# Kernel tuning notes

Measured on AMD Instinct MI355X. Metric: run time of the kernel, lower is better.

The kernel has to match this reference:

```python
import math
import jax, jax.numpy as jnp
from jax import lax
import numpy as np

B, H_IMG, W_IMG = 16, 512, 512
POOL, RATIO, SCALE = 23, 2, 0.25

def conv2d(x, w, b=None, stride=1, pad=0):
    y = lax.conv_general_dilated(x, w, (stride, stride), [(pad, pad), (pad, pad)],
                                 dimension_numbers=('NCHW', 'OIHW', 'NCHW'))
    return y if b is None else y + b[None, :, None, None]

def batchnorm(x, g, b, eps=1e-5):
    # training-mode BN (module is never put in eval mode): batch statistics
    m = x.mean((0, 2, 3), keepdims=True)
    v = x.var((0, 2, 3), keepdims=True)
    return g[None, :, None, None] * (x - m) * lax.rsqrt(v + eps) + b[None, :, None, None]

def maxpool(x, k, s, p=0):
    return lax.reduce_window(x, -jnp.inf, lax.max, (1, 1, k, k), (1, 1, s, s),
                             [(0, 0), (0, 0), (p, p), (p, p)])

def affine_grid(theta, H, W):
    # F.affine_grid, align_corners=False
    xs = (jnp.arange(W, dtype=jnp.float32) * 2 + 1) / W - 1
    ys = (jnp.arange(H, dtype=jnp.float32) * 2 + 1) / H - 1
    gx, gy = jnp.meshgrid(xs, ys)  # [H,W]
    base = jnp.stack([gx, gy, jnp.ones_like(gx)], axis=-1)  # [H,W,3]
    return base @ theta.T  # [H,W,2] -> (x,y) source coords

def grid_sample(imgs, grid):
    # bilinear, zero padding, align_corners=False; imgs [B,C,H,W], grid [H,W,2]
    _, C, H, W = imgs.shape
    ix = ((grid[..., 0] + 1) * W - 1) * 0.5
    iy = ((grid[..., 1] + 1) * H - 1) * 0.5
    x0, y0 = jnp.floor(ix), jnp.floor(iy)
    wa = (x0 + 1 - ix) * (y0 + 1 - iy)
    wb = (x0 + 1 - ix) * (iy - y0)
    wc = (ix - x0) * (y0 + 1 - iy)
    wd = (ix - x0) * (iy - y0)
    def gather(img, yy, xx):
        valid = (xx >= 0) & (xx < W) & (yy >= 0) & (yy < H)
        return img[:, jnp.clip(yy, 0, H - 1).astype(jnp.int32),
                      jnp.clip(xx, 0, W - 1).astype(jnp.int32)] * valid
    def one(img):
        return (gather(img, y0, x0) * wa + gather(img, y0 + 1, x0) * wb +
                gather(img, y0, x0 + 1) * wc + gather(img, y0 + 1, x0 + 1) * wd)
    return jax.vmap(one)(imgs)

def roialign(feat, ind, boxes):
    # torchvision ROIAlign(output=(23,23), spatial_scale=0.25, sampling_ratio=2, aligned=False)
    C, H, W = feat.shape[1:]
    x1, y1, x2, y2 = (boxes * SCALE).T
    bw = jnp.maximum(x2 - x1, 1.0) / POOL
    bh = jnp.maximum(y2 - y1, 1.0) / POOL
    off = (jnp.arange(RATIO, dtype=jnp.float32) + 0.5) / RATIO
    pos = (jnp.arange(POOL, dtype=jnp.float32)[:, None] + off[None, :]).reshape(-1)  # [46]
    ys = y1[:, None] + pos[None, :] * bh[:, None]  # [N,46]
    xs = x1[:, None] + pos[None, :] * bw[:, None]
    S = POOL * RATIO
    def one(img, yv, xv):
        empty = ((yv[:, None] < -1.0) | (yv[:, None] > H) |
                 (xv[None, :] < -1.0) | (xv[None, :] > W))  # [S,S]
        y = jnp.broadcast_to(jnp.clip(yv, 0.0, H - 1.0)[:, None], (S, S))
        x = jnp.broadcast_to(jnp.clip(xv, 0.0, W - 1.0)[None, :], (S, S))
        y0f, x0f = jnp.floor(y), jnp.floor(x)
        y0 = y0f.astype(jnp.int32); x0 = x0f.astype(jnp.int32)
        y1i = jnp.minimum(y0 + 1, H - 1); x1i = jnp.minimum(x0 + 1, W - 1)
        ly, lx = y - y0f, x - x0f
        hy, hx = 1.0 - ly, 1.0 - lx
        v = (img[:, y0, x0] * (hy * hx) + img[:, y0, x1i] * (hy * lx) +
             img[:, y1i, x0] * (ly * hx) + img[:, y1i, x1i] * (ly * lx))
        v = jnp.where(empty[None], 0.0, v)
        return v.reshape(C, POOL, RATIO, POOL, RATIO).mean((2, 4))
    return jax.vmap(one)(feat[ind], ys, xs)  # [N,C,23,23]

def forward(x, box, stem_w, stem_g, stem_b, conv1_w, conv1_b, bn1_g, bn1_b,
            conv2_w, conv2_b, fc1_w, fc1_b, head_w, head_b):
    x = x.transpose(0, 3, 1, 2)  # NHWC -> NCHW
    # resnet stem (7x7/2 conv + BN + ReLU + 3x3/2 maxpool): 64 ch @ stride 4
    f = maxpool(jax.nn.relu(batchnorm(conv2d(x, stem_w, stride=2, pad=3), stem_g, stem_b)), 3, 2, 1)
    Bc, C, H, W = f.shape
    a = -5 * math.pi / 180
    theta1 = jnp.array([[math.cos(a), math.sin(-a), 0.0], [math.sin(a), math.cos(a), 0.0]], jnp.float32)
    a = 5 * math.pi / 180
    theta2 = jnp.array([[math.cos(a), math.sin(-a), 0.0], [math.sin(a), math.cos(a), 0.0]], jnp.float32)
    xt1 = grid_sample(f, affine_grid(theta1, H, W))
    xt2 = grid_sample(f, affine_grid(theta2, H, W))
    ind = jnp.arange(Bc, dtype=jnp.int32)
    b7 = box.reshape(Bc, 7, 4)
    # focus1..focus7 on f, channel order matches torch.cat((f1..f7), dim=1)
    boxes7 = b7.transpose(1, 0, 2).reshape(7 * Bc, 4)
    f7 = roialign(f, jnp.tile(ind, 7), boxes7).reshape(7, Bc, C, POOL, POOL)
    f7 = f7.transpose(1, 0, 2, 3, 4).reshape(Bc, 7 * C, POOL, POOL)
    b1, b2 = b7[:, 0], b7[:, 1]
    f8 = roialign(xt1, ind, b1)
    f9 = roialign(xt1, ind, b2)
    f10 = roialign(xt2, ind, b1)
    f11 = roialign(xt2, ind, b2)
    h = jnp.concatenate([f7, f8, f9, f10, f11], axis=1)  # [B,704,23,23]
    h = maxpool(jax.nn.relu(batchnorm(conv2d(h, conv1_w, conv1_b), bn1_g, bn1_b)), 2, 2)  # [B,64,10,10]
    h = jax.nn.relu(conv2d(h, conv2_w, conv2_b))  # [B,32,8,8]
    h = h.reshape(Bc, 32 * 8 * 8)
    h = jax.nn.relu(h @ fc1_w.T + fc1_b)
    return jnp.tanh(h @ head_w.T + head_b)  # [B,12]

def setup_inputs() -> dict:
    key = jax.random.key(0)
    ks = jax.random.split(key, 8)
    x = jax.random.normal(ks[0], (B, H_IMG, W_IMG, 3), jnp.float32)
    xy = jax.random.uniform(ks[1], (B, 7, 2), jnp.float32, 0.0, 300.0)
    wh = jax.random.uniform(ks[2], (B, 7, 2), jnp.float32, 50.0, 200.0)
    box = jnp.concatenate([xy, xy + wh], axis=-1).reshape(B, 28)
    def w(k, shape, fan_in):
        return jax.random.normal(k, shape, jnp.float32) / np.float32(np.sqrt(fan_in))
    return dict(
        x=x, box=box,
        stem_w=w(ks[3], (64, 3, 7, 7), 3 * 49),
        stem_g=jnp.ones((64,), jnp.float32), stem_b=jnp.zeros((64,), jnp.float32),
        conv1_w=w(ks[4], (64, 704, 3, 3), 704 * 9), conv1_b=jnp.zeros((64,), jnp.float32),
        bn1_g=jnp.ones((64,), jnp.float32), bn1_b=jnp.zeros((64,), jnp.float32),
        conv2_w=w(ks[5], (32, 64, 3, 3), 64 * 9), conv2_b=jnp.zeros((32,), jnp.float32),
        fc1_w=w(ks[6], (128, 2048), 2048), fc1_b=jnp.zeros((128,), jnp.float32),
        head_w=w(ks[7], (12, 128), 128), head_b=jnp.zeros((12,), jnp.float32),
    )

def reference(x, box, stem_w, stem_g, stem_b, conv1_w, conv1_b, bn1_g, bn1_b,
              conv2_w, conv2_b, fc1_w, fc1_b, head_w, head_b):
    return forward(x, box, stem_w, stem_g, stem_b, conv1_w, conv1_b, bn1_g, bn1_b,
                   conv2_w, conv2_b, fc1_w, fc1_b, head_w, head_b)
```

## Files before the change

### kernel.cpp

```cpp
#include <hip/hip_runtime.h>
#include <hip/hip_bf16.h>


#define C5 0.9961946980917455f
#define S5 0.08715574274765817f

typedef __attribute__((ext_vector_type(8))) short short8;
typedef __attribute__((ext_vector_type(4))) float f32x4;

typedef __attribute__((address_space(3))) ushort lds_ushort;
typedef const __attribute__((address_space(1))) ushort gbl_ushort;

__device__ __forceinline__ ushort f2bf_bits(float v) {
    __hip_bfloat16 b = __float2bfloat16(v);
    ushort u;
    __builtin_memcpy(&u, &b, 2);
    return u;
}
__device__ __forceinline__ float bfbits2f(ushort u) {
    __hip_bfloat16 b;
    __builtin_memcpy(&b, &u, 2);
    return __bfloat162float(b);
}

__global__ __launch_bounds__(256) void k_cvtall(const float* __restrict__ x,
                                                ushort* __restrict__ xbf,
                                                const float* __restrict__ w1,
                                                __hip_bfloat16* __restrict__ w1b,
                                                const float* __restrict__ sw,
                                                __hip_bfloat16* __restrict__ w2b,
                                                float* __restrict__ stats_raw) {
    const int bx = blockIdx.x;
    if (bx < 12627) {
        const int t = bx * 256 + threadIdx.x;
        if (t >= 3232480) return;
        const int n = t / 202020;
        const int r = t - n * 202020;
        const int row = r / 390, col = r - row * 390;
        const int ih = row - 3;
        float4 v = {0.f, 0.f, 0.f, 0.f};
        if ((unsigned)ih < 512u && col >= 3 && col <= 386)
            v = *(const float4*)(x + (size_t)n * 786432 + (size_t)ih * 1536 + 4 * col - 12);
        uint2 p;
        p.x = (uint)f2bf_bits(v.x) | ((uint)f2bf_bits(v.y) << 16);
        p.y = (uint)f2bf_bits(v.z) | ((uint)f2bf_bits(v.w) << 16);
        *(uint2*)(xbf + 4 * (size_t)t) = p;
    } else {
        const int t = (bx - 12627) * 256 + threadIdx.x;
        if (t < 405504) {
            w1b[t] = __float2bfloat16(w1[t]);
        } else if (t < 417792) {
            const int e = t - 405504;
            const int oc = e / 192, k = e - oc * 192;
            const int kh = k / 24, u = k - kh * 24;
            float v = 0.f;
            if (u >= 3 && kh < 7) {
                int tt = u - 3;
                int kw = tt / 3, ci = tt - kw * 3;
                v = sw[oc * 147 + ci * 49 + kh * 7 + kw];
            }
            w2b[e] = __float2bfloat16(v);
        } else if (t < 417920) {
            stats_raw[t - 417792] = 0.f;
        }
    }
}

__global__ __launch_bounds__(64, 4) void k_stem(const ushort* __restrict__ xbf,
                                                const ushort* __restrict__ w2b,
                                                __hip_bfloat16* __restrict__ out) {
    __shared__ __align__(16) ushort lds[4608];
    const int bx = blockIdx.x;
    const int gi = ((bx & 7) << 11) + (bx >> 3);
    const int wq = gi & 3;
    const int oh = (gi >> 2) & 255;
    const int n  = gi >> 10;
    const int lane = threadIdx.x;
    const int quad = lane >> 4, m = lane & 15;
    const int p0 = wq * 64;

    {
        const ushort* src = xbf + (size_t)n * 808080 + (size_t)(oh * 2) * 1560 + 6 * p0;
        if (lane < 51) {
#pragma unroll
            for (int row = 0; row < 8; row++)
                __builtin_amdgcn_global_load_lds((gbl_ushort*)(src + row * 1560 + lane * 8),
                                                 (lds_ushort*)(lds + row * 416 + lane * 8),
                                                 16, 0, 0);
        }
    }
    asm volatile("s_waitcnt vmcnt(0)" ::: "memory");
    __builtin_amdgcn_sched_barrier(0);

    f32x4 acc[4][4] = {};
#pragma unroll
    for (int ks = 0; ks < 6; ks++) {
        const int g   = ks * 4 + quad;
        const int kh  = g / 3;
        const int gi2 = g - kh * 3;
        const uint* rr = (const uint*)lds + kh * 208 + 4 * gi2;
        short8 b[4];
#pragma unroll
        for (int nt = 0; nt < 4; nt++) {
            const uint* q = rr + 3 * (nt * 16 + m);
            uint4 t = (uint4){q[0], q[1], q[2], q[3]};
            __builtin_memcpy(&b[nt], &t, 16);
        }
        const int ko = ks * 32 + quad * 8;
#pragma unroll
        for (int mt = 0; mt < 4; mt++) {
            const short8 a = *(const short8*)(w2b + (size_t)(mt * 16 + m) * 192 + ko);
#pragma unroll
            for (int nt = 0; nt < 4; nt++)
                acc[mt][nt] = __builtin_amdgcn_mfma_f32_16x16x32_bf16(a, b[nt], acc[mt][nt], 0, 0, 0);
        }
    }

#pragma unroll
    for (int mt = 0; mt < 4; mt++)
#pragma unroll
        for (int nt = 0; nt < 4; nt++)
#pragma unroll
            for (int r = 0; r < 4; r++)
                lds[(mt * 16 + quad * 4 + r) * 72 + nt * 16 + m] = f2bf_bits(acc[mt][nt][r]);

    ushort* outb = (ushort*)out + (size_t)n * 64 * 65536 + oh * 256 + p0;
    const int ocl = lane >> 3, ch = lane & 7;
#pragma unroll
    for (int p = 0; p < 8; p++) {
        const int oc = p * 8 + ocl;
        uint4 v = *(const uint4*)&lds[oc * 72 + ch * 8];
        *(uint4*)(outb + (size_t)oc * 65536 + ch * 8) = v;
    }
}

__global__ __launch_bounds__(256) void k_sumstem(const ushort* __restrict__ stem,
                                                 float* __restrict__ stats_raw) {
    const int c = blockIdx.x >> 3, s = blockIdx.x & 7;
    const int tid = threadIdx.x;
    const uint4* b0 = (const uint4*)(stem + ((size_t)(s * 2) * 64 + c) * 65536);
    const uint4* b1 = (const uint4*)(stem + ((size_t)(s * 2 + 1) * 64 + c) * 65536);
    float sum = 0.f, sq = 0.f;
    for (int i = tid; i < 8192; i += 256) {
        uint4 v0 = b0[i], v1 = b1[i];
#pragma unroll
        for (int k = 0; k < 4; k++) {
            uint u0 = ((const uint*)&v0)[k], u1 = ((const uint*)&v1)[k];
            float a0 = __uint_as_float(u0 << 16);
            float a1 = __uint_as_float(u0 & 0xffff0000u);
            float a2 = __uint_as_float(u1 << 16);
            float a3 = __uint_as_float(u1 & 0xffff0000u);
            sum += a0 + a1 + a2 + a3;
            sq = fmaf(a0, a0, fmaf(a1, a1, fmaf(a2, a2, fmaf(a3, a3, sq))));
        }
    }
#pragma unroll
    for (int off = 32; off; off >>= 1) {
        sum += __shfl_xor(sum, off, 64);
        sq  += __shfl_xor(sq, off, 64);
    }
    __shared__ float shS[4], shQ[4];
    if ((tid & 63) == 0) { shS[tid >> 6] = sum; shQ[tid >> 6] = sq; }
    __syncthreads();
    if (tid == 0) {
        atomicAdd(&stats_raw[c * 2],     shS[0] + shS[1] + shS[2] + shS[3]);
        atomicAdd(&stats_raw[c * 2 + 1], shQ[0] + shQ[1] + shQ[2] + shQ[3]);
    }
}

__global__ __launch_bounds__(256) void k_bn1stats(const float* __restrict__ c1,
                                                  const float* __restrict__ gamma,
                                                  const float* __restrict__ beta,
                                                  float* __restrict__ stats1) {
    const int c = blockIdx.x;
    const int tid = threadIdx.x;
    float s = 0.f, ss = 0.f;
    for (int e = tid; e < 7056; e += 256) {
        int n = e / 441, p = e - n * 441;
        float v = c1[(n * 64 + c) * 441 + p];
        s += v; ss += v * v;
    }
    __shared__ float sh[8], sh2[8];
#pragma unroll
    for (int off = 32; off; off >>= 1) {
        s += __shfl_xor(s, off, 64);
        ss += __shfl_xor(ss, off, 64);
    }
    if ((tid & 63) == 0) { sh[tid >> 6] = s; sh2[tid >> 6] = ss; }
    __syncthreads();
    if (tid == 0) {
        s = sh[0] + sh[1] + sh[2] + sh[3];
        ss = sh2[0] + sh2[1] + sh2[2] + sh2[3];
        const float inv_n = 1.f / 7056.f;
        float mn = s * inv_n;
        float var = ss * inv_n - mn * mn;
        float a = gamma[c] * rsqrtf(var + 1e-5f);
        stats1[c] = a;
        stats1[64 + c] = beta[c] - mn * a;
    }
}

__global__ __launch_bounds__(256) void k_bnpool(const __hip_bfloat16* __restrict__ sin_,
                                                const float* __restrict__ stats_raw,
                                                const float* __restrict__ gamma,
                                                const float* __restrict__ beta,
                                                float* __restrict__ f) {
    const int idx = blockIdx.x * 256 + threadIdx.x;
    const int pwg = idx & 15;
    const int ph = (idx >> 4) & 127;
    const int c = (idx >> 11) & 63;
    const int n = idx >> 17;
    const int pw0 = pwg * 8;
    const float inv_n = 1.f / 1048576.f;
    const float S = stats_raw[c * 2], Q = stats_raw[c * 2 + 1];
    const float mn = S * inv_n;
    const float var = Q * inv_n - mn * mn;
    const float a = gamma[c] * rsqrtf(var + 1e-5f);
    const float b = beta[c] - mn * a;
    const uint* base = (const uint*)((const ushort*)sin_ + (size_t)(n * 64 + c) * 65536);

    float colmax[17];
#pragma unroll
    for (int k = 0; k < 17; k++) colmax[k] = -1e30f;

    const int r0 = ph * 2 - 1;
#pragma unroll
    for (int dr = 0; dr < 3; dr++) {
        const int r = r0 + dr;
        const bool rv = (unsigned)r < 256u;
        uint d[9];
        const uint* rp = base + r * 128 + pw0 - 1;
#pragma unroll
        for (int j = 0; j < 9; j++)
            d[j] = (rv && (pw0 > 0 || j > 0)) ? rp[j] : 0u;
#pragma unroll
        for (int j = 0; j < 9; j++) {
            float vhi = a * bfbits2f((ushort)(d[j] >> 16)) + b;
            colmax[2 * j] = rv ? fmaxf(colmax[2 * j], vhi) : colmax[2 * j];
            if (j > 0) {
                float vlo = a * bfbits2f((ushort)(d[j] & 0xFFFFu)) + b;
                colmax[2 * j - 1] = rv ? fmaxf(colmax[2 * j - 1], vlo) : colmax[2 * j - 1];
            }
        }
    }
    if (pw0 == 0) colmax[0] = -1e30f;

    float o[8];
#pragma unroll
    for (int i = 0; i < 8; i++)
        o[i] = fmaxf(fmaxf(colmax[2 * i], fmaxf(colmax[2 * i + 1], colmax[2 * i + 2])), 0.f);
    float* fp = f + (size_t)(n * 64 + c) * 16384 + ph * 128 + pw0;
    *(float4*)fp       = (float4){o[0], o[1], o[2], o[3]};
    *(float4*)(fp + 4) = (float4){o[4], o[5], o[6], o[7]};
}

__device__ __forceinline__ float gs_pad(const float* band, int ry0g,
                                        float ix, float iy) {
    float x0f = floorf(ix), y0f = floorf(iy);
    float lx = ix - x0f, ly = iy - y0f;
    float hx = 1.f - lx, hy = 1.f - ly;
    const int base = ((int)y0f - ry0g) * 144 + (int)x0f + 8;
    return band[base] * (hx * hy) + band[base + 144] * (hx * ly)
         + band[base + 1] * (lx * hy) + band[base + 145] * (lx * ly);
}

__global__ __launch_bounds__(256, 3) void k_gridsample2(const float* __restrict__ f,
                                                        float* __restrict__ xt1,
                                                        float* __restrict__ xt2) {
    __shared__ float band[78 * 144];
    const int bx = blockIdx.x;
    const int half = bx & 1;
    const int img_i = bx >> 1;
    const int h0 = half * 64;
    const int ry0g = half ? 57 : -7;
    const float* img = f + (size_t)img_i * 16384;
    const int tid = threadIdx.x;
    for (int e = tid; e < 78 * 36; e += 256) {
        const int r = e / 36, q = e - r * 36;
        const int gr = ry0g + r;
        float4 v = {0.f, 0.f, 0.f, 0.f};
        if ((unsigned)gr < 128u && q >= 2 && q <= 33)
            v = *(const float4*)(img + gr * 128 + 4 * q - 8);
        ((float4*)band)[e] = v;
    }
    __syncthreads();

    float* o1 = xt1 + (size_t)img_i * 16384 + h0 * 128;
    float* o2 = xt2 + (size_t)img_i * 16384 + h0 * 128;
    for (int e = tid; e < 8192; e += 256) {
        const int h = h0 + (e >> 7);
        const int w = e & 127;
        float gx = (2 * w + 1) * (1.f / 128.f) - 1.f;
        float gy = (2 * h + 1) * (1.f / 128.f) - 1.f;
        float g0a = C5 * gx + S5 * gy,  g1a = -S5 * gx + C5 * gy;
        float g0b = C5 * gx - S5 * gy,  g1b =  S5 * gx + C5 * gy;
        o1[e] = gs_pad(band, ry0g, ((g0a + 1.f) * 128.f - 1.f) * 0.5f,
                                   ((g1a + 1.f) * 128.f - 1.f) * 0.5f);
        o2[e] = gs_pad(band, ry0g, ((g0b + 1.f) * 128.f - 1.f) * 0.5f,
                                   ((g1b + 1.f) * 128.f - 1.f) * 0.5f);
    }
}

__global__ __launch_bounds__(256) void k_roialign(const float* __restrict__ f,
                                                  const float* __restrict__ xt1,
                                                  const float* __restrict__ xt2,
                                                  const float* __restrict__ box,
                                                  __hip_bfloat16* __restrict__ h) {
    __shared__ float reg[52 * 53];
    const int bx = blockIdx.x;
    const int job = bx % 11;
    const int nc = bx / 11;
    const int c = nc & 63;
    const int n = nc >> 6;
    int j, cbase;
    const float* src;
    if (job < 7)      { j = job;     cbase = job * 64;             src = f;   }
    else if (job < 9) { j = job - 7; cbase = 448 + (job - 7) * 64; src = xt1; }
    else              { j = job - 9; cbase = 576 + (job - 9) * 64; src = xt2; }
    const float* bp = box + n * 28 + j * 4;
    const float x1 = bp[0] * 0.25f, y1 = bp[1] * 0.25f;
    const float x2 = bp[2] * 0.25f, y2 = bp[3] * 0.25f;
    const float bw = fmaxf(x2 - x1, 1.f) * (1.f / 23.f);
    const float bh = fmaxf(y2 - y1, 1.f) * (1.f / 23.f);

    const int ry0 = (int)floorf(fminf(fmaxf(y1 + 0.25f * bh, 0.f), 127.f));
    int ry1 = min((int)floorf(fminf(fmaxf(y1 + 22.75f * bh, 0.f), 127.f)) + 1, 127);
    ry1 = min(ry1, ry0 + 51);
    const int rx0 = (int)floorf(fminf(fmaxf(x1 + 0.25f * bw, 0.f), 127.f));
    int rx1 = min((int)floorf(fminf(fmaxf(x1 + 22.75f * bw, 0.f), 127.f)) + 1, 127);
    rx1 = min(rx1, rx0 + 51);
    const int RH = ry1 - ry0 + 1, RW = rx1 - rx0 + 1;

    const float* img = src + (size_t)(n * 64 + c) * 16384;
    const int tid = threadIdx.x;
    const int lane = tid & 63, wv = tid >> 6;
    for (int r = wv; r < RH; r += 4)
        if (lane < RW)
            reg[r * 53 + lane] = img[(ry0 + r) * 128 + rx0 + lane];
    __syncthreads();

    __hip_bfloat16* hb = h + (size_t)(n * 704 + cbase + c) * 529;
    for (int pp = tid; pp < 529; pp += 256) {
        const int ph = pp / 23, pw = pp - ph * 23;
        float sum = 0.f;
#pragma unroll
        for (int s = 0; s < 4; s++) {
            const int r1 = s >> 1, r2 = s & 1;
            const float yv = y1 + (ph + r1 * 0.5f + 0.25f) * bh;
            const float xv = x1 + (pw + r2 * 0.5f + 0.25f) * bw;
            const bool ok = !(yv < -1.f || yv > 128.f || xv < -1.f || xv > 128.f);
            float y = fminf(fmaxf(yv, 0.f), 127.f);
            float x = fminf(fmaxf(xv, 0.f), 127.f);
            float y0f = floorf(y), x0f = floorf(x);
            int y0 = (int)y0f, x0 = (int)x0f;
            int iy0 = y0 - ry0, ix0 = x0 - rx0;
            int iy1 = min(y0 + 1, 127) - ry0, ix1 = min(x0 + 1, 127) - rx0;
            float ly = y - y0f, lx = x - x0f;
            float hy = 1.f - ly, hx = 1.f - lx;
            const float sc = ok ? 1.f : 0.f;
            sum += sc * (reg[iy0 * 53 + ix0] * (hy * hx) + reg[iy0 * 53 + ix1] * (hy * lx)
                       + reg[iy1 * 53 + ix0] * (ly * hx) + reg[iy1 * 53 + ix1] * (ly * lx));
        }
        hb[pp] = __float2bfloat16(sum * 0.25f);
    }
}

__global__ __launch_bounds__(256) void k_conv1m(const ushort* __restrict__ hb,
                                                const ushort* __restrict__ w1b,
                                                float* __restrict__ c1p) {
    __shared__ __align__(16) ushort Bs[2][2][32][40];
    const int bx = blockIdx.x;
    const int pt = bx % 17;
    const int n  = (bx / 17) & 15;
    const int s  = bx / 272;
    const int tid = threadIdx.x;
    const int w = tid >> 6, lane = tid & 63;
    const int quad = lane >> 4, m = lane & 15;
    const int kbase = s * 704;
    const int posb = pt * 32;
    const size_t hb_n = (size_t)n * 704 * 529;
    f32x4 acc0 = {0.f, 0.f, 0.f, 0.f};
    f32x4 acc1 = {0.f, 0.f, 0.f, 0.f};
    const ushort* wrow = w1b + (size_t)(w * 16 + m) * 6336;

    int ep[8], ek[8], epos[8];
#pragma unroll
    for (int i = 0; i < 8; i++) {
        const int e = tid + 256 * i;
        ep[i] = e >> 10; ek[i] = (e >> 5) & 31; epos[i] = e & 31;
    }
    ushort rbuf[8];
#pragma unroll
    for (int i = 0; i < 8; i++) {
        const int k = kbase + ep[i] * 32 + ek[i];
        const int ci = k / 9, tap = k - ci * 9;
        const int kh = tap / 3, kw = tap - kh * 3;
        rbuf[i] = hb[hb_n + (size_t)ci * 529 + kh * 23 + kw + posb + epos[i]];
    }
#pragma unroll
    for (int i = 0; i < 8; i++) Bs[0][ep[i]][epos[i]][ek[i]] = rbuf[i];

    for (int it = 0; it < 11; it++) {
        __syncthreads();
        const int cur = it & 1;
        if (it < 10) {
            const int k0 = kbase + (it + 1) * 64;
#pragma unroll
            for (int i = 0; i < 8; i++) {
                const int k = k0 + ep[i] * 32 + ek[i];
                const int ci = k / 9, tap = k - ci * 9;
                const int kh = tap / 3, kw = tap - kh * 3;
                rbuf[i] = hb[hb_n + (size_t)ci * 529 + kh * 23 + kw + posb + epos[i]];
            }
        }
        const int k0 = kbase + it * 64;
        const short8 a0  = *(const short8*)(wrow + k0 + quad * 8);
        const short8 a1  = *(const short8*)(wrow + k0 + 32 + quad * 8);
        const short8 b00 = *(const short8*)&Bs[cur][0][m][quad * 8];
        const short8 b01 = *(const short8*)&Bs[cur][0][16 + m][quad * 8];
        const short8 b10 = *(const short8*)&Bs[cur][1][m][quad * 8];
        const short8 b11 = *(const short8*)&Bs[cur][1][16 + m][quad * 8];
        acc0 = __builtin_amdgcn_mfma_f32_16x16x32_bf16(a0, b00, acc0, 0, 0, 0);
        acc1 = __builtin_amdgcn_mfma_f32_16x16x32_bf16(a0, b01, acc1, 0, 0, 0);
        acc0 = __builtin_amdgcn_mfma_f32_16x16x32_bf16(a1, b10, acc0, 0, 0, 0);
        acc1 = __builtin_amdgcn_mfma_f32_16x16x32_bf16(a1, b11, acc1, 0, 0, 0);
        if (it < 10) {
#pragma unroll
            for (int i = 0; i < 8; i++) Bs[cur ^ 1][ep[i]][epos[i]][ek[i]] = rbuf[i];
        }
    }
    float* outp = c1p + ((size_t)(s * 16 + n) * 64) * 544;
#pragma unroll
    for (int r = 0; r < 4; r++) {
        const int oc = w * 16 + quad * 4 + r;
        outp[(size_t)oc * 544 + posb + m]      = acc0[r];
        outp[(size_t)oc * 544 + posb + 16 + m] = acc1[r];
    }
}

__global__ __launch_bounds__(256) void k_c1red(const float* __restrict__ c1p,
                                               const float* __restrict__ b1,
                                               float* __restrict__ c1) {
    const int t = blockIdx.x * 256 + threadIdx.x;
    const int p = t % 441;
    const int oc = (t / 441) % 64;
    const int n = t / 28224;
    const int ph = p / 21, pw = p - ph * 21;
    const int p529 = ph * 23 + pw;
    const size_t base = ((size_t)n * 64 + oc) * 544 + p529;
    const size_t sstr = (size_t)16 * 64 * 544;
    float v = 0.f;
#pragma unroll
    for (int k = 0; k < 9; k++) v += c1p[base + k * sstr];
    c1[t] = v + b1[oc];
}

__global__ __launch_bounds__(256) void k_bnpool2(const float* __restrict__ c1,
                                                 const float* __restrict__ stats1,
                                                 float* __restrict__ p1) {
    const int t = blockIdx.x * 256 + threadIdx.x;
    const int pw = t % 10;
    const int ph = (t / 10) % 10;
    const int c = (t / 100) % 64;
    const int n = t / 6400;
    const float a = stats1[c], b = stats1[64 + c];
    const float* base = c1 + (size_t)(n * 64 + c) * 441;
    const int r = ph * 2, cc = pw * 2;
    float v0 = a * base[r * 21 + cc] + b;
    float v1 = a * base[r * 21 + cc + 1] + b;
    float v2 = a * base[(r + 1) * 21 + cc] + b;
    float v3 = a * base[(r + 1) * 21 + cc + 1] + b;
    p1[t] = fmaxf(fmaxf(fmaxf(v0, v1), fmaxf(v2, v3)), 0.f);
}

__global__ __launch_bounds__(256) void k_conv2(const float* __restrict__ p1,
                                               const float* __restrict__ w2,
                                               const float* __restrict__ b2,
                                               float* __restrict__ c2) {
    __shared__ float ip[6400];
    __shared__ float wl[2304];
    const int bx = blockIdx.x;
    const int n = bx >> 3, ocq = bx & 7;
    const int tid = threadIdx.x;
    const float4* p14 = (const float4*)(p1 + (size_t)n * 6400);
    float4* ip4 = (float4*)ip;
    for (int e = tid; e < 1600; e += 256) ip4[e] = p14[e];
    for (int e = tid; e < 2304; e += 256) wl[e] = w2[ocq * 2304 + e];
    __syncthreads();

    const int ocl = tid >> 6, pos = tid & 63;
    const int ph = pos >> 3, pw = pos & 7;
    const int oc = ocq * 4 + ocl;
    float s = b2[oc];
    const float* wb = wl + ocl * 576;
    const float* ib = ip + ph * 10 + pw;
    for (int ci = 0; ci < 64; ci++) {
        const float* r = ib + ci * 100;
        const float* ww = wb + ci * 9;
        s += r[0] * ww[0] + r[1] * ww[1] + r[2] * ww[2]
           + r[10] * ww[3] + r[11] * ww[4] + r[12] * ww[5]
           + r[20] * ww[6] + r[21] * ww[7] + r[22] * ww[8];
    }
    c2[(size_t)(n * 32 + oc) * 64 + pos] = fmaxf(s, 0.f);
}

__global__ __launch_bounds__(64) void k_fc1(const float* __restrict__ c2,
                                            const float* __restrict__ fw,
                                            const float* __restrict__ fb,
                                            float* __restrict__ fo) {
    const int bx = blockIdx.x;
    const int oc = bx & 127, n = bx >> 7;
    const int lane = threadIdx.x;
    const float* a = c2 + (size_t)n * 2048;
    const float* w = fw + (size_t)oc * 2048;
    float s = 0.f;
    for (int k = lane; k < 2048; k += 64) s += a[k] * w[k];
#pragma unroll
    for (int off = 32; off; off >>= 1) s += __shfl_xor(s, off, 64);
    if (lane == 0) fo[n * 128 + oc] = fmaxf(s + fb[oc], 0.f);
}

__global__ __launch_bounds__(64) void k_head(const float* __restrict__ fo,
                                             const float* __restrict__ hw,
                                             const float* __restrict__ hb,
                                             float* __restrict__ out) {
    const int bx = blockIdx.x;
    const int oc = bx % 12, n = bx / 12;
    const int lane = threadIdx.x;
    float s = 0.f;
    for (int k = lane; k < 128; k += 64) s += fo[n * 128 + k] * hw[oc * 128 + k];
#pragma unroll
    for (int off = 32; off; off >>= 1) s += __shfl_xor(s, off, 64);
    if (lane == 0) out[bx] = tanhf(s + hb[oc]);
}

extern "C" void kernel_launch(void* const* d_in, const int* in_sizes, int n_in,
                              void* d_out, int out_size, void* d_ws, size_t ws_size,
                              hipStream_t stream) {
    const float* x       = (const float*)d_in[0];
    const float* box     = (const float*)d_in[1];
    const float* stem_w  = (const float*)d_in[2];
    const float* stem_g  = (const float*)d_in[3];
    const float* stem_b  = (const float*)d_in[4];
    const float* conv1_w = (const float*)d_in[5];
    const float* conv1_b = (const float*)d_in[6];
    const float* bn1_g   = (const float*)d_in[7];
    const float* bn1_b   = (const float*)d_in[8];
    const float* conv2_w = (const float*)d_in[9];
    const float* conv2_b = (const float*)d_in[10];
    const float* fc1_w   = (const float*)d_in[11];
    const float* fc1_b   = (const float*)d_in[12];
    const float* head_w  = (const float*)d_in[13];
    const float* head_b  = (const float*)d_in[14];
    float* out = (float*)d_out;
    float* w = (float*)d_ws;

    const size_t F_SZ = 16777216;
    float* f   = w;
    ushort* xbf = (ushort*)w;
    float* c1p = w;
    __hip_bfloat16* stem = (__hip_bfloat16*)(w + F_SZ);
    float* xt1 = w + F_SZ;
    float* xt2 = w + 2 * F_SZ;
    float* base3 = w + 3 * F_SZ;
    __hip_bfloat16* hbuf = (__hip_bfloat16*)base3;
    float* c1   = base3 + 2979392;
    float* p1   = c1 + 451584;
    float* c2   = p1 + 102400;
    float* fo   = c2 + 32768;
    float* stats_raw = fo + 2048;
    float* stats1  = stats_raw + 128;
    __hip_bfloat16* w1b = (__hip_bfloat16*)(stats1 + 128);
    __hip_bfloat16* w2b = (__hip_bfloat16*)(stats1 + 128 + 202752);

    k_cvtall<<<14263, 256, 0, stream>>>(x, xbf, conv1_w, w1b, stem_w, w2b, stats_raw);
    k_stem<<<16384, 64, 0, stream>>>(xbf, (const ushort*)w2b, stem);
    k_sumstem<<<512, 256, 0, stream>>>((const ushort*)stem, stats_raw);
    k_bnpool<<<8192, 256, 0, stream>>>(stem, stats_raw, stem_g, stem_b, f);
    k_gridsample2<<<2048, 256, 0, stream>>>(f, xt1, xt2);
    k_roialign<<<11264, 256, 0, stream>>>(f, xt1, xt2, box, hbuf);
    k_conv1m<<<2448, 256, 0, stream>>>((const ushort*)hbuf, (const ushort*)w1b, c1p);
    k_c1red<<<1764, 256, 0, stream>>>(c1p, conv1_b, c1);
    k_bn1stats<<<64, 256, 0, stream>>>(c1, bn1_g, bn1_b, stats1);
    k_bnpool2<<<400, 256, 0, stream>>>(c1, stats1, p1);
    k_conv2<<<128, 256, 0, stream>>>(p1, conv2_w, conv2_b, c2);
    k_fc1<<<2048, 64, 0, stream>>>(c2, fc1_w, fc1_b, fo);
    k_head<<<192, 64, 0, stream>>>(fo, head_w, head_b, out);
}
```

Before: 416.2 us.

## Fuse rotation grid-sample into ROIAlign, computing rotated features only inside box regions

Drops the full-image grid-sample kernel, which wrote two rotated copies of the whole feature map, and fuses the rotation into a new ROIAlign kernel. For each box it loads only the bounding source patch into LDS, builds the rotated region in LDS, then pools from it. This removes the large intermediate write and read and avoids computing rotated pixels outside the boxes. The source patch is capped at 60x60, which could clip coverage if a box's rotated extent were larger.

```diff
diff --git a/kernel.cpp b/kernel.cpp
--- a/kernel.cpp
+++ b/kernel.cpp
@@ -254,69 +254,16 @@
     *(float4*)(fp + 4) = (float4){o[4], o[5], o[6], o[7]};
 }
 
-__device__ __forceinline__ float gs_pad(const float* band, int ry0g,
-                                        float ix, float iy) {
-    float x0f = floorf(ix), y0f = floorf(iy);
-    float lx = ix - x0f, ly = iy - y0f;
-    float hx = 1.f - lx, hy = 1.f - ly;
-    const int base = ((int)y0f - ry0g) * 144 + (int)x0f + 8;
-    return band[base] * (hx * hy) + band[base + 144] * (hx * ly)
-         + band[base + 1] * (lx * hy) + band[base + 145] * (lx * ly);
-}
-
-__global__ __launch_bounds__(256, 3) void k_gridsample2(const float* __restrict__ f,
-                                                        float* __restrict__ xt1,
-                                                        float* __restrict__ xt2) {
-    __shared__ float band[78 * 144];
-    const int bx = blockIdx.x;
-    const int half = bx & 1;
-    const int img_i = bx >> 1;
-    const int h0 = half * 64;
-    const int ry0g = half ? 57 : -7;
-    const float* img = f + (size_t)img_i * 16384;
-    const int tid = threadIdx.x;
-    for (int e = tid; e < 78 * 36; e += 256) {
-        const int r = e / 36, q = e - r * 36;
-        const int gr = ry0g + r;
-        float4 v = {0.f, 0.f, 0.f, 0.f};
-        if ((unsigned)gr < 128u && q >= 2 && q <= 33)
-            v = *(const float4*)(img + gr * 128 + 4 * q - 8);
-        ((float4*)band)[e] = v;
-    }
-    __syncthreads();
-
-    float* o1 = xt1 + (size_t)img_i * 16384 + h0 * 128;
-    float* o2 = xt2 + (size_t)img_i * 16384 + h0 * 128;
-    for (int e = tid; e < 8192; e += 256) {
-        const int h = h0 + (e >> 7);
-        const int w = e & 127;
-        float gx = (2 * w + 1) * (1.f / 128.f) - 1.f;
-        float gy = (2 * h + 1) * (1.f / 128.f) - 1.f;
-        float g0a = C5 * gx + S5 * gy,  g1a = -S5 * gx + C5 * gy;
-        float g0b = C5 * gx - S5 * gy,  g1b =  S5 * gx + C5 * gy;
-        o1[e] = gs_pad(band, ry0g, ((g0a + 1.f) * 128.f - 1.f) * 0.5f,
-                                   ((g1a + 1.f) * 128.f - 1.f) * 0.5f);
-        o2[e] = gs_pad(band, ry0g, ((g0b + 1.f) * 128.f - 1.f) * 0.5f,
-                                   ((g1b + 1.f) * 128.f - 1.f) * 0.5f);
-    }
-}
-
-__global__ __launch_bounds__(256) void k_roialign(const float* __restrict__ f,
-                                                  const float* __restrict__ xt1,
-                                                  const float* __restrict__ xt2,
-                                                  const float* __restrict__ box,
-                                                  __hip_bfloat16* __restrict__ h) {
+__global__ __launch_bounds__(256) void k_roialign_f(const float* __restrict__ f,
+                                                    const float* __restrict__ box,
+                                                    __hip_bfloat16* __restrict__ h) {
     __shared__ float reg[52 * 53];
     const int bx = blockIdx.x;
-    const int job = bx % 11;
-    const int nc = bx / 11;
+    const int job = bx % 7;
+    const int nc = bx / 7;
     const int c = nc & 63;
     const int n = nc >> 6;
-    int j, cbase;
-    const float* src;
-    if (job < 7)      { j = job;     cbase = job * 64;             src = f;   }
-    else if (job < 9) { j = job - 7; cbase = 448 + (job - 7) * 64; src = xt1; }
-    else              { j = job - 9; cbase = 576 + (job - 9) * 64; src = xt2; }
+    const int j = job, cbase = job * 64;
     const float* bp = box + n * 28 + j * 4;
     const float x1 = bp[0] * 0.25f, y1 = bp[1] * 0.25f;
     const float x2 = bp[2] * 0.25f, y2 = bp[3] * 0.25f;
@@ -331,7 +278,7 @@
     rx1 = min(rx1, rx0 + 51);
     const int RH = ry1 - ry0 + 1, RW = rx1 - rx0 + 1;
 
-    const float* img = src + (size_t)(n * 64 + c) * 16384;
+    const float* img = f + (size_t)(n * 64 + c) * 16384;
     const int tid = threadIdx.x;
     const int lane = tid & 63, wv = tid >> 6;
     for (int r = wv; r < RH; r += 4)
@@ -360,6 +307,124 @@
             const float sc = ok ? 1.f : 0.f;
             sum += sc * (reg[iy0 * 53 + ix0] * (hy * hx) + reg[iy0 * 53 + ix1] * (hy * lx)
                        + reg[iy1 * 53 + ix0] * (ly * hx) + reg[iy1 * 53 + ix1] * (ly * lx));
+        }
+        hb[pp] = __float2bfloat16(sum * 0.25f);
+    }
+}
+
+__device__ __forceinline__ float bt_tap(const float* ft, int sy0, int sx0,
+                                        int nr, int nc2,
+                                        float yy, float xx, float wt) {
+    bool valid = (xx >= 0.f) & (xx < 128.f) & (yy >= 0.f) & (yy < 128.f);
+    int xi = (int)fminf(fmaxf(xx, 0.f), 127.f);
+    int yi = (int)fminf(fmaxf(yy, 0.f), 127.f);
+    int r = min(max(yi - sy0, 0), nr - 1);
+    int cc = min(max(xi - sx0, 0), nc2 - 1);
+    return valid ? ft[r * 61 + cc] * wt : 0.f;
+}
+
+__global__ __launch_bounds__(256) void k_roialign_rot(const float* __restrict__ f,
+                                                      const float* __restrict__ box,
+                                                      __hip_bfloat16* __restrict__ h) {
+    __shared__ float ft[60 * 61];
+    __shared__ float xtt[52 * 53];
+    const int bx = blockIdx.x;
+    const int jr = bx & 3;
+    const int nc = bx >> 2;
+    const int c = nc & 63;
+    const int n = nc >> 6;
+    const float s5 = (jr >> 1) ? -S5 : S5;
+    const int j = jr & 1;
+    const int cbase = 448 + jr * 64;
+    const float* bp = box + n * 28 + j * 4;
+    const float x1 = bp[0] * 0.25f, y1 = bp[1] * 0.25f;
+    const float x2 = bp[2] * 0.25f, y2 = bp[3] * 0.25f;
+    const float bw = fmaxf(x2 - x1, 1.f) * (1.f / 23.f);
+    const float bh = fmaxf(y2 - y1, 1.f) * (1.f / 23.f);
+
+    const int ry0 = (int)floorf(fminf(fmaxf(y1 + 0.25f * bh, 0.f), 127.f));
+    int ry1 = min((int)floorf(fminf(fmaxf(y1 + 22.75f * bh, 0.f), 127.f)) + 1, 127);
+    ry1 = min(ry1, ry0 + 51);
+    const int rx0 = (int)floorf(fminf(fmaxf(x1 + 0.25f * bw, 0.f), 127.f));
+    int rx1 = min((int)floorf(fminf(fmaxf(x1 + 22.75f * bw, 0.f), 127.f)) + 1, 127);
+    rx1 = min(rx1, rx0 + 51);
+    const int RH = ry1 - ry0 + 1, RW = rx1 - rx0 + 1;
+
+    const float gxa = (2 * rx0 + 1) * (1.f / 128.f) - 1.f;
+    const float gxb = (2 * rx1 + 1) * (1.f / 128.f) - 1.f;
+    const float gya = (2 * ry0 + 1) * (1.f / 128.f) - 1.f;
+    const float gyb = (2 * ry1 + 1) * (1.f / 128.f) - 1.f;
+    float ixm = 1e30f, ixM = -1e30f, iym = 1e30f, iyM = -1e30f;
+#pragma unroll
+    for (int k = 0; k < 4; k++) {
+        const float gx = (k & 1) ? gxb : gxa;
+        const float gy = (k & 2) ? gyb : gya;
+        const float g0 = C5 * gx + s5 * gy;
+        const float g1 = -s5 * gx + C5 * gy;
+        const float ix = ((g0 + 1.f) * 128.f - 1.f) * 0.5f;
+        const float iy = ((g1 + 1.f) * 128.f - 1.f) * 0.5f;
+        ixm = fminf(ixm, ix); ixM = fmaxf(ixM, ix);
+        iym = fminf(iym, iy); iyM = fmaxf(iyM, iy);
+    }
+    const int sx0 = max(0, (int)floorf(fminf(fmaxf(ixm, 0.f), 127.f)) - 1);
+    int sx1 = min(127, (int)floorf(fminf(fmaxf(ixM, 0.f), 127.f)) + 2);
+    sx1 = min(sx1, sx0 + 59);
+    const int sy0 = max(0, (int)floorf(fminf(fmaxf(iym, 0.f), 127.f)) - 1);
+    int sy1 = min(127, (int)floorf(fminf(fmaxf(iyM, 0.f), 127.f)) + 2);
+    sy1 = min(sy1, sy0 + 59);
+    const int RH2 = sy1 - sy0 + 1, RW2 = sx1 - sx0 + 1;
+
+    const float* img = f + (size_t)(n * 64 + c) * 16384;
+    const int tid = threadIdx.x;
+    const int lane = tid & 63, wv = tid >> 6;
+    for (int r = wv; r < RH2; r += 4)
+        if (lane < RW2)
+            ft[r * 61 + lane] = img[(sy0 + r) * 128 + sx0 + lane];
+    __syncthreads();
+
+    for (int e = tid; e < RH * RW; e += 256) {
+        const int r = e / RW, cw = e - r * RW;
+        const int hh = ry0 + r, ww = rx0 + cw;
+        const float gx = (2 * ww + 1) * (1.f / 128.f) - 1.f;
+        const float gy = (2 * hh + 1) * (1.f / 128.f) - 1.f;
+        const float g0 = C5 * gx + s5 * gy;
+        const float g1 = -s5 * gx + C5 * gy;
+        const float ix = ((g0 + 1.f) * 128.f - 1.f) * 0.5f;
+        const float iy = ((g1 + 1.f) * 128.f - 1.f) * 0.5f;
+        const float x0f = floorf(ix), y0f = floorf(iy);
+        const float lx = ix - x0f, ly = iy - y0f;
+        const float wa = (1.f - lx) * (1.f - ly);
+        const float wb = (1.f - lx) * ly;
+        const float wc = lx * (1.f - ly);
+        const float wd = lx * ly;
+        xtt[r * 53 + cw] = bt_tap(ft, sy0, sx0, RH2, RW2, y0f,       x0f,       wa)
+                         + bt_tap(ft, sy0, sx0, RH2, RW2, y0f + 1.f, x0f,       wb)
+                         + bt_tap(ft, sy0, sx0, RH2, RW2, y0f,       x0f + 1.f, wc)
+                         + bt_tap(ft, sy0, sx0, RH2, RW2, y0f + 1.f, x0f + 1.f, wd);
+    }
+    __syncthreads();
+
+    __hip_bfloat16* hb = h + (size_t)(n * 704 + cbase + c) * 529;
+    for (int pp = tid; pp < 529; pp += 256) {
+        const int ph = pp / 23, pw = pp - ph * 23;
+        float sum = 0.f;
+#pragma unroll
+        for (int s = 0; s < 4; s++) {
+            const int r1 = s >> 1, r2 = s & 1;
+            const float yv = y1 + (ph + r1 * 0.5f + 0.25f) * bh;
+            const float xv = x1 + (pw + r2 * 0.5f + 0.25f) * bw;
+            const bool ok = !(yv < -1.f || yv > 128.f || xv < -1.f || xv > 128.f);
+            float y = fminf(fmaxf(yv, 0.f), 127.f);
+            float x = fminf(fmaxf(xv, 0.f), 127.f);
+            float y0f = floorf(y), x0f = floorf(x);
+            int y0 = (int)y0f, x0 = (int)x0f;
+            int iy0 = y0 - ry0, ix0 = x0 - rx0;
+            int iy1 = min(y0 + 1, 127) - ry0, ix1 = min(x0 + 1, 127) - rx0;
+            float ly = y - y0f, lx = x - x0f;
+            float hy = 1.f - ly, hx = 1.f - lx;
+            const float sc = ok ? 1.f : 0.f;
+            sum += sc * (xtt[iy0 * 53 + ix0] * (hy * hx) + xtt[iy0 * 53 + ix1] * (hy * lx)
+                       + xtt[iy1 * 53 + ix0] * (ly * hx) + xtt[iy1 * 53 + ix1] * (ly * lx));
         }
         hb[pp] = __float2bfloat16(sum * 0.25f);
     }
@@ -560,8 +625,6 @@
     ushort* xbf = (ushort*)w;
     float* c1p = w;
     __hip_bfloat16* stem = (__hip_bfloat16*)(w + F_SZ);
-    float* xt1 = w + F_SZ;
-    float* xt2 = w + 2 * F_SZ;
     float* base3 = w + 3 * F_SZ;
     __hip_bfloat16* hbuf = (__hip_bfloat16*)base3;
     float* c1   = base3 + 2979392;
@@ -577,8 +640,8 @@
     k_stem<<<16384, 64, 0, stream>>>(xbf, (const ushort*)w2b, stem);
     k_sumstem<<<512, 256, 0, stream>>>((const ushort*)stem, stats_raw);
     k_bnpool<<<8192, 256, 0, stream>>>(stem, stats_raw, stem_g, stem_b, f);
-    k_gridsample2<<<2048, 256, 0, stream>>>(f, xt1, xt2);
-    k_roialign<<<11264, 256, 0, stream>>>(f, xt1, xt2, box, hbuf);
+    k_roialign_f<<<7168, 256, 0, stream>>>(f, box, hbuf);
+    k_roialign_rot<<<4096, 256, 0, stream>>>(f, box, hbuf);
     k_conv1m<<<2448, 256, 0, stream>>>((const ushort*)hbuf, (const ushort*)w1b, c1p);
     k_c1red<<<1764, 256, 0, stream>>>(c1p, conv1_b, c1);
     k_bn1stats<<<64, 256, 0, stream>>>(c1, bn1_g, bn1_b, stats1);
```

Result: faster. 399.5 us (-4.0%).
